# Kernel tuning notes

Hardware: AMD Instinct MI355X
Metric: run time of the kernel (lower is better)

The kernel has to match this reference:

```python
import jax, jax.numpy as jnp
import numpy as np

B, N, D, H, L = 2, 2048, 128, 8, 3
V = 32          # NUM_ATOM_TYPES (assumed)
DH = D // H
SCALE = 1.0 / (DH ** 0.5)
NEG = -1e9      # stands in for -inf in the additive attention mask
EPS = 1e-5


def _ln(x, g, b):
    m = x.mean(-1, keepdims=True)
    v = ((x - m) ** 2).mean(-1, keepdims=True)
    return (x - m) / jnp.sqrt(v + EPS) * g + b


def setup_inputs() -> dict:
    key = jax.random.key(0)
    ks = jax.random.split(key, 24)
    nrm = lambda k, shape, std=0.02: jax.random.normal(k, shape, jnp.float32) * std
    atom_embed = nrm(ks[0], (V, D)).at[0].set(0.0)  # padding_idx = 0
    cons_embed = nrm(ks[1], (1, 1, D))
    in_w = nrm(ks[2], (D, D)); in_b = jnp.zeros((D,), jnp.float32)
    qkv_w = nrm(ks[3], (L, 3 * D, D)); qkv_b = jnp.zeros((L, 3 * D), jnp.float32)
    out_w = nrm(ks[4], (L, D, D)); out_b = jnp.zeros((L, D), jnp.float32)
    ln1_g = jnp.ones((L, D), jnp.float32); ln1_b = jnp.zeros((L, D), jnp.float32)
    ln2_g = jnp.ones((L, D), jnp.float32); ln2_b = jnp.zeros((L, D), jnp.float32)
    ff1_w = nrm(ks[5], (L, 4 * D, D)); ff1_b = jnp.zeros((L, 4 * D), jnp.float32)
    ff2_w = nrm(ks[6], (L, D, 4 * D)); ff2_b = jnp.zeros((L, D), jnp.float32)
    struct_bias = nrm(ks[7], (L,), 0.5)  # scalar per layer (init 0 in torch; randomized to exercise the path)
    head_ln_g = jnp.ones((D,), jnp.float32); head_ln_b = jnp.zeros((D,), jnp.float32)
    head_w = nrm(ks[8], (1, D)); head_b = jnp.zeros((1,), jnp.float32)
    is_atom = jax.random.bernoulli(ks[9], 0.5, (B, N))
    atom_id = jax.random.randint(ks[10], (B, N), 0, V)
    mask = jax.random.bernoulli(ks[11], 0.9, (B, N))
    adjacency = (jax.random.uniform(ks[12], (B, N, N)) < 0.002).astype(jnp.float32)
    adjacency = jnp.maximum(adjacency, jnp.eye(N, dtype=jnp.float32)[None])  # self-loops
    root_idx = jax.random.randint(ks[13], (B,), 0, N)
    return dict(atom_embed=atom_embed, cons_embed=cons_embed, in_w=in_w, in_b=in_b,
                qkv_w=qkv_w, qkv_b=qkv_b, out_w=out_w, out_b=out_b,
                ln1_g=ln1_g, ln1_b=ln1_b, ln2_g=ln2_g, ln2_b=ln2_b,
                ff1_w=ff1_w, ff1_b=ff1_b, ff2_w=ff2_w, ff2_b=ff2_b,
                struct_bias=struct_bias, head_ln_g=head_ln_g, head_ln_b=head_ln_b,
                head_w=head_w, head_b=head_b, adjacency=adjacency,
                is_atom=is_atom, atom_id=atom_id, mask=mask, root_idx=root_idx)


def reference(atom_embed, cons_embed, in_w, in_b, qkv_w, qkv_b, out_w, out_b,
              ln1_g, ln1_b, ln2_g, ln2_b, ff1_w, ff1_b, ff2_w, ff2_b,
              struct_bias, head_ln_g, head_ln_b, head_w, head_b,
              adjacency, is_atom, atom_id, mask, root_idx):
    # node embeddings
    ae = atom_embed[jnp.clip(atom_id, 0, V - 1)]                     # [B,N,D]
    h = jnp.where(is_atom[..., None], ae, jnp.broadcast_to(cons_embed, (B, N, D)))
    h = h @ in_w.T + in_b
    # additive attention mask: valid pairs OK; invalid query rows attend only to self
    pair_ok = mask[:, :, None] & mask[:, None, :]
    eye = jnp.eye(N, dtype=bool)[None]
    ok = pair_ok | ((~mask)[:, :, None] & eye)
    am = jnp.where(ok, 0.0, NEG).astype(jnp.float32)                 # [B,N,N]
    for i in range(L):
        x = _ln(h, ln1_g[i], ln1_b[i])
        qkv = (x @ qkv_w[i].T + qkv_b[i]).reshape(B, N, 3, H, DH)
        q, k, v = (jnp.transpose(qkv[:, :, j], (0, 2, 1, 3)) for j in range(3))  # [B,H,N,DH]
        scores = jnp.einsum('bhqd,bhkd->bhqk', q, k) * SCALE \
                 + struct_bias[i] * adjacency[:, None] + am[:, None]
        attn = jax.nn.softmax(scores, axis=-1)
        o = jnp.einsum('bhqk,bhkd->bhqd', attn, v)
        o = jnp.transpose(o, (0, 2, 1, 3)).reshape(B, N, D)
        h = h + (o @ out_w[i].T + out_b[i])
        x2 = _ln(h, ln2_g[i], ln2_b[i])
        f = jax.nn.gelu(x2 @ ff1_w[i].T + ff1_b[i], approximate=False)
        h = h + (f @ ff2_w[i].T + ff2_b[i])
    pooled = h[jnp.arange(B), root_idx]                              # [B,D]
    p = _ln(pooled, head_ln_g, head_ln_b)
    return (p @ head_w.T + head_b)[:, 0]                             # [B]
```

## Files before the change

### kernel.cpp

```cpp
#include <hip/hip_runtime.h>
#include <cmath>

#define NB 2
#define NN 2048
#define ND 128
#define NH 8
#define NL 3
#define NV 32
#define NDH 16
#define LN_EPS 1e-5f
#define QSCALE 0.36067376022224085f

typedef __bf16 bf8_t __attribute__((ext_vector_type(8)));
typedef __bf16 bf4_t __attribute__((ext_vector_type(4)));
typedef float f4x __attribute__((ext_vector_type(4)));
typedef float f16x __attribute__((ext_vector_type(16)));

struct CastArgs {
  const float* s[5];
  __bf16* d[5];
  int startblk[5];
};
__global__ __launch_bounds__(256) void prep_kernel(
    CastArgs a, const float* __restrict__ adj, unsigned long long* __restrict__ abits,
    const int* __restrict__ mask, unsigned long long* __restrict__ mbits) {
  int blk = blockIdx.x;
  int lane = threadIdx.x & 63;
  if (blk < 592) {
    int seg = 0;
#pragma unroll
    for (int i = 1; i < 5; i++) seg += (blk >= a.startblk[i]) ? 1 : 0;
    int i4 = (blk - a.startblk[seg]) * 256 + threadIdx.x;
    float4 v = ((const float4*)a.s[seg])[i4];
    bf4_t p = {(__bf16)v.x, (__bf16)v.y, (__bf16)v.z, (__bf16)v.w};
    ((bf4_t*)a.d[seg])[i4] = p;
  } else if (blk < 592 + 8192) {
    int g = ((blk - 592) * 4 + (threadIdx.x >> 6)) * 4;
    const float* p = adj + (size_t)g * 64 + lane;
    unsigned long long w0 = __ballot(p[0] != 0.0f);
    unsigned long long w1 = __ballot(p[64] != 0.0f);
    unsigned long long w2 = __ballot(p[128] != 0.0f);
    unsigned long long w3 = __ballot(p[192] != 0.0f);
    if (lane == 0) {
      abits[g] = w0; abits[g + 1] = w1; abits[g + 2] = w2; abits[g + 3] = w3;
    }
  } else {
    int g = (blk - 8784) * 4 + (threadIdx.x >> 6);
    int v = mask[g * 64 + lane];
    unsigned long long bal = __ballot(v != 0);
    if (lane == 0) mbits[g] = bal;
  }
}

__global__ __launch_bounds__(512) void fused0_kernel(
    const float* __restrict__ atom_embed, const float* __restrict__ cons_embed,
    const int* __restrict__ is_atom, const int* __restrict__ atom_id,
    const __bf16* __restrict__ W1, const float* __restrict__ b1,
    float* __restrict__ Hout,
    const float* __restrict__ lng, const float* __restrict__ lnb,
    const __bf16* __restrict__ W2, const float* __restrict__ b2,
    __bf16* __restrict__ Qb, __bf16* __restrict__ Kb, __bf16* __restrict__ Vt) {
  __shared__ __bf16 Xs[16][136];
  __shared__ __bf16 Ws[128][136];
  __shared__ float Hs[16][132];
  __shared__ __bf16 X2[16][136];
  int m0 = blockIdx.x * 16;
  int g = blockIdx.y;
  int t = threadIdx.x;
  int lane = t & 63, w = t >> 6;
  int l15 = lane & 15, quad = lane >> 4;
  const int NC2 = (g == 0) ? 2 : 1;
  const int T = 1 + NC2;

  {
    int r = t >> 5, c = t & 31;
    int row = m0 + r;
    int id = atom_id[row];
    id = id < 0 ? 0 : (id > NV - 1 ? NV - 1 : id);
    const float* src = is_atom[row] ? (atom_embed + (size_t)id * ND) : cons_embed;
    float4 v = *(const float4*)&src[c * 4];
    bf4_t p = {(__bf16)v.x, (__bf16)v.y, (__bf16)v.z, (__bf16)v.w};
    *(bf4_t*)&Xs[r][c * 4] = p;
  }

  bf8_t wreg[4];
  auto issue = [&](int i) {
    const __bf16* base;
    int rowoff;
    if (i == 0) { base = W1; rowoff = 0; }
    else {
      int nc = (g == 0) ? (i - 1) : 2;
      base = W2; rowoff = nc * 128;
    }
#pragma unroll
    for (int jj = 0; jj < 4; jj++) {
      int c = t + jj * 512;
      wreg[jj] = *(const bf8_t*)&base[(size_t)(rowoff + (c >> 4)) * 128 + (c & 15) * 8];
    }
  };
  issue(0);

  for (int i = 0; i < T; i++) {
    if (i) __syncthreads();
#pragma unroll
    for (int jj = 0; jj < 4; jj++) {
      int c = t + jj * 512;
      *(bf8_t*)&Ws[c >> 4][(c & 15) * 8] = wreg[jj];
    }
    __syncthreads();
    if (i + 1 < T) issue(i + 1);
    if (i == 0) {
      f4x a1 = {0.f, 0.f, 0.f, 0.f};
#pragma unroll
      for (int kk = 0; kk < 4; kk++) {
        bf8_t a = *(const bf8_t*)&Xs[l15][kk * 32 + quad * 8];
        bf8_t b = *(const bf8_t*)&Ws[w * 16 + l15][kk * 32 + quad * 8];
        a1 = __builtin_amdgcn_mfma_f32_16x16x32_bf16(a, b, a1, 0, 0, 0);
      }
      int n = w * 16 + l15;
      float bv = b1[n];
#pragma unroll
      for (int r = 0; r < 4; r++) {
        int m = quad * 4 + r;
        float v = a1[r] + bv;
        if (g == 0) Hout[(size_t)(m0 + m) * ND + n] = v;
        Hs[m][n] = v;
      }
      __syncthreads();
      {
        int r = t >> 5, c = t & 31;
        float4 v = *(const float4*)&Hs[r][c * 4];
        float s1 = v.x + v.y + v.z + v.w;
        float s2 = v.x * v.x + v.y * v.y + v.z * v.z + v.w * v.w;
#pragma unroll
        for (int m = 16; m >= 1; m >>= 1) {
          s1 += __shfl_xor(s1, m, 64);
          s2 += __shfl_xor(s2, m, 64);
        }
        float mean = s1 * (1.0f / ND);
        float var = s2 * (1.0f / ND) - mean * mean;
        float rstd = rsqrtf(var + LN_EPS);
        float4 gg = *(const float4*)&lng[c * 4];
        float4 bb = *(const float4*)&lnb[c * 4];
        bf4_t p;
        p[0] = (__bf16)((v.x - mean) * rstd * gg.x + bb.x);
        p[1] = (__bf16)((v.y - mean) * rstd * gg.y + bb.y);
        p[2] = (__bf16)((v.z - mean) * rstd * gg.z + bb.z);
        p[3] = (__bf16)((v.w - mean) * rstd * gg.w + bb.w);
        *(bf4_t*)&X2[r][c * 4] = p;
      }
    } else {
      int nc = (g == 0) ? (i - 1) : 2;
      f4x a2 = {0.f, 0.f, 0.f, 0.f};
#pragma unroll
      for (int kk = 0; kk < 4; kk++) {
        bf8_t a = *(const bf8_t*)&X2[l15][kk * 32 + quad * 8];
        bf8_t b = *(const bf8_t*)&Ws[w * 16 + l15][kk * 32 + quad * 8];
        a2 = __builtin_amdgcn_mfma_f32_16x16x32_bf16(a, b, a2, 0, 0, 0);
      }
      int n = nc * 128 + w * 16 + l15;
      float bv = b2[n];
#pragma unroll
      for (int r = 0; r < 4; r++) {
        int m = m0 + quad * 4 + r;
        float v = a2[r] + bv;
        if (n < ND) Qb[(size_t)m * ND + n] = (__bf16)(v * QSCALE);
        else if (n < 2 * ND) Kb[(size_t)m * ND + n - ND] = (__bf16)v;
        else {
          int c2 = n - 2 * ND, hh = c2 >> 4, d0 = c2 & 15;
          int bb2 = m >> 11, nn = m & 2047;
          Vt[((size_t)((bb2 * NH + hh) * NDH + d0)) * NN + nn] = (__bf16)v;
        }
      }
    }
  }
}

template <int LAST>
__global__ __launch_bounds__(512) void layer_kernel(
    const __bf16* __restrict__ Ob,
    const __bf16* __restrict__ Wout, const float* __restrict__ bout,
    const float* __restrict__ Hin, float* __restrict__ Hout,
    const float* __restrict__ ln2g, const float* __restrict__ ln2b,
    const __bf16* __restrict__ Wff1, const float* __restrict__ bff1,
    const __bf16* __restrict__ Wff2, const float* __restrict__ bff2,
    const float* __restrict__ ln1g, const float* __restrict__ ln1b,
    const __bf16* __restrict__ Wqkv, const float* __restrict__ bqkv,
    __bf16* __restrict__ Qb, __bf16* __restrict__ Kb, __bf16* __restrict__ Vt,
    const int* __restrict__ root_idx, const float* __restrict__ hg,
    const float* __restrict__ hbt, const float* __restrict__ hwp,
    const float* __restrict__ hbp, float* __restrict__ outp) {
  __shared__ __bf16 Xs[16][136];
  __shared__ __bf16 Ws[128][136];
  __shared__ float Hs[16][132];
  __shared__ __bf16 X2[16][136];
  __shared__ __bf16 Fs[16][520];
  int m0 = blockIdx.x * 16;
  int g = blockIdx.y;
  int t = threadIdx.x;
  int lane = t & 63, w = t >> 6;
  int l15 = lane & 15, quad = lane >> 4;
  const int NQ = LAST ? 0 : (g == 0 ? 2 : 1);
  const int T = 9 + NQ;

  {
    int r = t >> 5, c = t & 31;
    *(bf4_t*)&Xs[r][c * 4] = *(const bf4_t*)&Ob[(size_t)(m0 + r) * ND + c * 4];
  }

  bf8_t wreg[4];
  auto issue = [&](int i) {
    const __bf16* base;
    int stride, rowoff, coloff;
    if (i == 0)     { base = Wout; stride = 128; rowoff = 0;             coloff = 0; }
    else if (i < 5) { base = Wff1; stride = 128; rowoff = (i - 1) * 128; coloff = 0; }
    else if (i < 9) { base = Wff2; stride = 512; rowoff = 0;             coloff = (i - 5) * 128; }
    else            { int nc = (g == 0) ? (i - 9) : 2;
                      base = Wqkv; stride = 128; rowoff = nc * 128;      coloff = 0; }
#pragma unroll
    for (int jj = 0; jj < 4; jj++) {
      int c = t + jj * 512;
      wreg[jj] = *(const bf8_t*)&base[(size_t)(rowoff + (c >> 4)) * stride + coloff + (c & 15) * 8];
    }
  };
  issue(0);

  auto do_ln = [&](const float* g_, const float* b_) {
    int r = t >> 5, c = t & 31;
    float4 v = *(const float4*)&Hs[r][c * 4];
    float s1 = v.x + v.y + v.z + v.w;
    float s2 = v.x * v.x + v.y * v.y + v.z * v.z + v.w * v.w;
#pragma unroll
    for (int m = 16; m >= 1; m >>= 1) {
      s1 += __shfl_xor(s1, m, 64);
      s2 += __shfl_xor(s2, m, 64);
    }
    float mean = s1 * (1.0f / ND);
    float var = s2 * (1.0f / ND) - mean * mean;
    float rstd = rsqrtf(var + LN_EPS);
    float4 gg = *(const float4*)&g_[c * 4];
    float4 bb = *(const float4*)&b_[c * 4];
    bf4_t p;
    p[0] = (__bf16)((v.x - mean) * rstd * gg.x + bb.x);
    p[1] = (__bf16)((v.y - mean) * rstd * gg.y + bb.y);
    p[2] = (__bf16)((v.z - mean) * rstd * gg.z + bb.z);
    p[3] = (__bf16)((v.w - mean) * rstd * gg.w + bb.w);
    *(bf4_t*)&X2[r][c * 4] = p;
  };

  f4x acc2 = {0.f, 0.f, 0.f, 0.f};
  for (int i = 0; i < T; i++) {
    if (i) __syncthreads();
#pragma unroll
    for (int jj = 0; jj < 4; jj++) {
      int c = t + jj * 512;
      *(bf8_t*)&Ws[c >> 4][(c & 15) * 8] = wreg[jj];
    }
    __syncthreads();
    if (i + 1 < T) issue(i + 1);
    if (i == 0) {
      f4x a1 = {0.f, 0.f, 0.f, 0.f};
#pragma unroll
      for (int kk = 0; kk < 4; kk++) {
        bf8_t a = *(const bf8_t*)&Xs[l15][kk * 32 + quad * 8];
        bf8_t b = *(const bf8_t*)&Ws[w * 16 + l15][kk * 32 + quad * 8];
        a1 = __builtin_amdgcn_mfma_f32_16x16x32_bf16(a, b, a1, 0, 0, 0);
      }
      int n = w * 16 + l15;
      float bv = bout[n];
#pragma unroll
      for (int r = 0; r < 4; r++) {
        int m = quad * 4 + r;
        Hs[m][n] = a1[r] + bv + Hin[(size_t)(m0 + m) * ND + n];
      }
      __syncthreads();
      do_ln(ln2g, ln2b);
    } else if (i < 5) {
      int c = i - 1;
      f4x a1 = {0.f, 0.f, 0.f, 0.f};
#pragma unroll
      for (int kk = 0; kk < 4; kk++) {
        bf8_t a = *(const bf8_t*)&X2[l15][kk * 32 + quad * 8];
        bf8_t b = *(const bf8_t*)&Ws[w * 16 + l15][kk * 32 + quad * 8];
        a1 = __builtin_amdgcn_mfma_f32_16x16x32_bf16(a, b, a1, 0, 0, 0);
      }
      int n = w * 16 + l15;
      float bv = bff1[c * 128 + n];
#pragma unroll
      for (int r = 0; r < 4; r++) {
        float v = a1[r] + bv;
        v = 0.5f * v * (1.0f + erff(v * 0.70710678118f));
        Fs[quad * 4 + r][c * 128 + n] = (__bf16)v;
      }
    } else if (i < 9) {
      int j = i - 5;
#pragma unroll
      for (int kk = 0; kk < 4; kk++) {
        bf8_t a = *(const bf8_t*)&Fs[l15][j * 128 + kk * 32 + quad * 8];
        bf8_t b = *(const bf8_t*)&Ws[w * 16 + l15][kk * 32 + quad * 8];
        acc2 = __builtin_amdgcn_mfma_f32_16x16x32_bf16(a, b, acc2, 0, 0, 0);
      }
      if (j == 3) {
        int n = w * 16 + l15;
        float bv = bff2[n];
#pragma unroll
        for (int r = 0; r < 4; r++) {
          int m = quad * 4 + r;
          float v = acc2[r] + bv + Hs[m][n];
          Hs[m][n] = v;
          if (g == 0) Hout[(size_t)(m0 + m) * ND + n] = v;
        }
        __syncthreads();
        if constexpr (!LAST) do_ln(ln1g, ln1b);
      }
    } else {
      int nc = (g == 0) ? (i - 9) : 2;
      f4x a2 = {0.f, 0.f, 0.f, 0.f};
#pragma unroll
      for (int kk = 0; kk < 4; kk++) {
        bf8_t a = *(const bf8_t*)&X2[l15][kk * 32 + quad * 8];
        bf8_t b = *(const bf8_t*)&Ws[w * 16 + l15][kk * 32 + quad * 8];
        a2 = __builtin_amdgcn_mfma_f32_16x16x32_bf16(a, b, a2, 0, 0, 0);
      }
      int n = nc * 128 + w * 16 + l15;
      float bv = bqkv[n];
#pragma unroll
      for (int r = 0; r < 4; r++) {
        int m = m0 + quad * 4 + r;
        float v = a2[r] + bv;
        if (n < ND) Qb[(size_t)m * ND + n] = (__bf16)(v * QSCALE);
        else if (n < 2 * ND) Kb[(size_t)m * ND + n - ND] = (__bf16)v;
        else {
          int c2 = n - 2 * ND, hh = c2 >> 4, d0 = c2 & 15;
          int bb2 = m >> 11, nn = m & 2047;
          Vt[((size_t)((bb2 * NH + hh) * NDH + d0)) * NN + nn] = (__bf16)v;
        }
      }
    }
  }

  if constexpr (LAST) {
    if (w < NB) {
      int rt = root_idx[w];
      int rglob = w * NN + rt;
      if (rglob >= m0 && rglob < m0 + 16) {
        int r = rglob - m0;
        float v0 = Hs[r][2 * lane], v1 = Hs[r][2 * lane + 1];
        float s1 = v0 + v1, s2 = v0 * v0 + v1 * v1;
#pragma unroll
        for (int m = 32; m >= 1; m >>= 1) {
          s1 += __shfl_xor(s1, m, 64);
          s2 += __shfl_xor(s2, m, 64);
        }
        float mean = s1 * (1.0f / ND);
        float var = s2 * (1.0f / ND) - mean * mean;
        float rstd = rsqrtf(var + LN_EPS);
        float p0 = (v0 - mean) * rstd * hg[2 * lane] + hbt[2 * lane];
        float p1 = (v1 - mean) * rstd * hg[2 * lane + 1] + hbt[2 * lane + 1];
        float part = p0 * hwp[2 * lane] + p1 * hwp[2 * lane + 1];
#pragma unroll
        for (int m = 32; m >= 1; m >>= 1) part += __shfl_xor(part, m, 64);
        if (lane == 0) outp[w] = part + hbp[0];
      }
    }
  }
}

__global__ __launch_bounds__(512) void attn_kernel(
    const __bf16* __restrict__ Qb, const __bf16* __restrict__ Kb,
    const __bf16* __restrict__ Vt, const unsigned int* __restrict__ adjbits,
    const unsigned int* __restrict__ maskbits, const int* __restrict__ mask,
    const float* __restrict__ sbias, int layer, __bf16* __restrict__ o) {
  int b = blockIdx.z, hh = blockIdx.y, q0 = blockIdx.x * 32;
  int wave = threadIdx.x >> 6;
  int lane = threadIdx.x & 63;
  int l31 = lane & 31, hi = lane >> 5;
  int l15 = lane & 15, quad = lane >> 4;
  float esb = __expf(sbias[layer]);
  const int bN = b * NN;
  const int kw0 = wave * 256;

  __shared__ __bf16 Pbuf[8][32][40];
  __shared__ float Ored[8][32][17];
  __shared__ float Lred[8][32];

  bf8_t Qf = *(const bf8_t*)(Qb + (size_t)(bN + q0 + l31) * ND + hh * NDH + hi * 8);

  int q = q0 + l31;
  int mq = mask[bN + q];
  const unsigned int* adjp = adjbits + (size_t)(bN + q) * (NN / 32) + (kw0 >> 5);
  const unsigned int* mbp = maskbits + (bN + kw0) / 32;
  const __bf16* kp = Kb + (size_t)(bN + kw0 + l31) * ND + hh * NDH + hi * 8;
  const __bf16* vp = Vt + (size_t)((b * NH + hh) * NDH + l15) * NN + kw0 + quad * 8;

  int dq = q - kw0;
  int tsel = dq >> 5;
  unsigned int selfw = 1u << (dq & 31);
  int sh4 = hi * 4;

  f4x Olo = {0.f, 0.f, 0.f, 0.f}, Ohi = {0.f, 0.f, 0.f, 0.f};
  float ls = 0.f;

  bf8_t Kf = *(const bf8_t*)kp;
  bf8_t Vf = *(const bf8_t*)vp;
  unsigned int aw = adjp[0];
  unsigned int mkw = mbp[0];

  for (int t = 0; t < 8; t++) {
    bf8_t Kn = Kf, Vn = Vf;
    unsigned int awn = aw, mkn = mkw;
    if (t < 7) {
      kp += 32 * ND;
      Kn = *(const bf8_t*)kp;
      Vn = *(const bf8_t*)(vp + (t + 1) * 32);
      awn = adjp[t + 1];
      mkn = mbp[t + 1];
    }
    f16x S = {0.f, 0.f, 0.f, 0.f, 0.f, 0.f, 0.f, 0.f,
              0.f, 0.f, 0.f, 0.f, 0.f, 0.f, 0.f, 0.f};
    S = __builtin_amdgcn_mfma_f32_32x32x16_bf16(Kf, Qf, S, 0, 0, 0);
    unsigned int okw = mq ? mkw : ((t == tsel) ? selfw : 0u);
    unsigned int wa = (aw & okw) >> sh4;
    unsigned int okh = okw >> sh4;
#pragma unroll
    for (int gg = 0; gg < 4; gg++) {
      bf4_t pk;
#pragma unroll
      for (int r = 0; r < 4; r++) {
        int c = gg * 8 + r;
        float e = __builtin_amdgcn_exp2f(S[gg * 4 + r]);
        float wgt = ((wa >> c) & 1) ? esb : (((okh >> c) & 1) ? 1.0f : 0.0f);
        float p = e * wgt;
        ls += p;
        pk[r] = (__bf16)p;
      }
      *(bf4_t*)&Pbuf[wave][l31][sh4 + gg * 8] = pk;
    }
    asm volatile("s_waitcnt lgkmcnt(0)" ::: "memory");
    bf8_t Plo = *(const bf8_t*)&Pbuf[wave][l15][quad * 8];
    bf8_t Phi = *(const bf8_t*)&Pbuf[wave][16 + l15][quad * 8];
    Olo = __builtin_amdgcn_mfma_f32_16x16x32_bf16(Plo, Vf, Olo, 0, 0, 0);
    Ohi = __builtin_amdgcn_mfma_f32_16x16x32_bf16(Phi, Vf, Ohi, 0, 0, 0);
    Kf = Kn; Vf = Vn; aw = awn; mkw = mkn;
  }

  ls += __shfl_xor(ls, 32, 64);
  if (hi == 0) Lred[wave][l31] = ls;
#pragma unroll
  for (int r = 0; r < 4; r++) {
    Ored[wave][quad * 4 + r][l15] = Olo[r];
    Ored[wave][16 + quad * 4 + r][l15] = Ohi[r];
  }
  __syncthreads();
  int row = threadIdx.x >> 4, col = threadIdx.x & 15;
  float s = 0.f, L = 0.f;
#pragma unroll
  for (int p = 0; p < 8; p++) {
    s += Ored[p][row][col];
    L += Lred[p][row];
  }
  o[(size_t)(bN + q0 + row) * ND + hh * NDH + col] = (__bf16)(s / L);
}

extern "C" void kernel_launch(void* const* d_in, const int* in_sizes, int n_in,
                              void* d_out, int out_size, void* d_ws, size_t ws_size,
                              hipStream_t stream) {
  const float* atom_embed = (const float*)d_in[0];
  const float* cons_embed = (const float*)d_in[1];
  const float* in_w  = (const float*)d_in[2];
  const float* in_b  = (const float*)d_in[3];
  const float* qkv_w = (const float*)d_in[4];
  const float* qkv_b = (const float*)d_in[5];
  const float* out_w = (const float*)d_in[6];
  const float* out_b = (const float*)d_in[7];
  const float* ln1_g = (const float*)d_in[8];
  const float* ln1_b = (const float*)d_in[9];
// ... 17 lines not shown

  const int MR = NB * NN;
  float* hA = (float*)d_ws;
  float* hB = hA + MR * ND;
  __bf16* Qb   = (__bf16*)(hB + MR * ND);
  __bf16* Kb   = Qb + MR * ND;
  __bf16* Vt   = Kb + MR * ND;
  __bf16* wbin = Vt + MR * ND;
  __bf16* wbqkv= wbin + ND * ND;
  __bf16* wbout= wbqkv + NL * 384 * ND;
  __bf16* wbff1= wbout + NL * ND * ND;
  __bf16* wbff2= wbff1 + NL * 512 * ND;
  unsigned int* adjb = (unsigned int*)(wbff2 + NL * ND * 512);
  unsigned int* mskb = adjb + NB * NN * NN / 32;
  __bf16* ob = (__bf16*)(mskb + 128);

  CastArgs ca;
  ca.s[0] = in_w;  ca.d[0] = wbin;  ca.startblk[0] = 0;
  ca.s[1] = qkv_w; ca.d[1] = wbqkv; ca.startblk[1] = 16;
  ca.s[2] = out_w; ca.d[2] = wbout; ca.startblk[2] = 160;
  ca.s[3] = ff1_w; ca.d[3] = wbff1; ca.startblk[3] = 208;
  ca.s[4] = ff2_w; ca.d[4] = wbff2; ca.startblk[4] = 400;
  prep_kernel<<<8800, 256, 0, stream>>>(ca, adj, (unsigned long long*)adjb,
                                        mask, (unsigned long long*)mskb);

  fused0_kernel<<<dim3(MR / 16, 2), 512, 0, stream>>>(
      atom_embed, cons_embed, is_atom, atom_id,
      wbin, in_b, hA, ln1_g, ln1_b, wbqkv, qkv_b, Qb, Kb, Vt);

  const float* hin[3]  = {hA, hB, hA};
  float* hout[3]       = {hB, hA, hB};
  for (int i = 0; i < NL; i++) {
    attn_kernel<<<dim3(NN / 32, NH, NB), 512, 0, stream>>>(
        Qb, Kb, Vt, adjb, mskb, mask, sbias, i, ob);
    if (i < NL - 1) {
      layer_kernel<0><<<dim3(MR / 16, 2), 512, 0, stream>>>(
          ob, wbout + (size_t)i * ND * ND, out_b + i * ND, hin[i], hout[i],
          ln2_g + i * ND, ln2_b + i * ND,
          wbff1 + (size_t)i * 512 * ND, ff1_b + i * 512,
          wbff2 + (size_t)i * ND * 512, ff2_b + i * ND,
          ln1_g + (i + 1) * ND, ln1_b + (i + 1) * ND,
          wbqkv + (size_t)(i + 1) * 384 * ND, qkv_b + (i + 1) * 384,
          Qb, Kb, Vt,
          nullptr, nullptr, nullptr, nullptr, nullptr, nullptr);
    } else {
      layer_kernel<1><<<dim3(MR / 16, 1), 512, 0, stream>>>(
          ob, wbout + (size_t)i * ND * ND, out_b + i * ND, hin[i], hout[i],
          ln2_g + i * ND, ln2_b + i * ND,
          wbff1 + (size_t)i * 512 * ND, ff1_b + i * 512,
          wbff2 + (size_t)i * ND * 512, ff2_b + i * ND,
          nullptr, nullptr, nullptr, nullptr,
          nullptr, nullptr, nullptr,
          root_idx, hg, hbt, hw, hb, out);
    }
  }
}
```

Before: 261.6 us.

## Fuse all layer kernels into one persistent megakernel with grid barriers

Replaces the separate fused0, attention and per-layer MLP kernel launches with a single persistent kernel of 512 blocks. The stages are separated by software grid barriers built on atomic counters, which prep_kernel zeroes. Each block handles two attention tiles and its share of the row-wise GEMM work per phase, reusing one dynamic shared memory buffer. The aim is to remove launch overhead and the gaps between kernels. The cost is barrier spin time, co-residency assumptions (512 blocks must all be resident), and possibly lower occupancy per phase.

Result: slower. 575.8 us (+120.1%).

```diff
diff --git a/kernel.cpp b/kernel.cpp
--- a/kernel.cpp
+++ b/kernel.cpp
@@ -10,6 +10,8 @@
 #define NDH 16
 #define LN_EPS 1e-5f
 #define QSCALE 0.36067376022224085f
+#define NBLK 512
+#define SMEM_BYTES 68608
 
 typedef __bf16 bf8_t __attribute__((ext_vector_type(8)));
 typedef __bf16 bf4_t __attribute__((ext_vector_type(4)));
@@ -23,9 +25,11 @@
 };
 __global__ __launch_bounds__(256) void prep_kernel(
     CastArgs a, const float* __restrict__ adj, unsigned long long* __restrict__ abits,
-    const int* __restrict__ mask, unsigned long long* __restrict__ mbits) {
+    const int* __restrict__ mask, unsigned long long* __restrict__ mbits,
+    unsigned* __restrict__ bars) {
   int blk = blockIdx.x;
   int lane = threadIdx.x & 63;
+  if (blk == 0 && threadIdx.x < 16) bars[threadIdx.x] = 0u;
   if (blk < 592) {
     int seg = 0;
 #pragma unroll
@@ -52,178 +56,56 @@
   }
 }
 
-__global__ __launch_bounds__(512) void fused0_kernel(
-    const float* __restrict__ atom_embed, const float* __restrict__ cons_embed,
-    const int* __restrict__ is_atom, const int* __restrict__ atom_id,
-    const __bf16* __restrict__ W1, const float* __restrict__ b1,
-    float* __restrict__ Hout,
-    const float* __restrict__ lng, const float* __restrict__ lnb,
-    const __bf16* __restrict__ W2, const float* __restrict__ b2,
-    __bf16* __restrict__ Qb, __bf16* __restrict__ Kb, __bf16* __restrict__ Vt) {
-  __shared__ __bf16 Xs[16][136];
-  __shared__ __bf16 Ws[128][136];
-  __shared__ float Hs[16][132];
-  __shared__ __bf16 X2[16][136];
-  int m0 = blockIdx.x * 16;
-  int g = blockIdx.y;
-  int t = threadIdx.x;
-  int lane = t & 63, w = t >> 6;
-  int l15 = lane & 15, quad = lane >> 4;
-  const int NC2 = (g == 0) ? 2 : 1;
-  const int T = 1 + NC2;
-
-  {
-    int r = t >> 5, c = t & 31;
-    int row = m0 + r;
-    int id = atom_id[row];
-    id = id < 0 ? 0 : (id > NV - 1 ? NV - 1 : id);
-    const float* src = is_atom[row] ? (atom_embed + (size_t)id * ND) : cons_embed;
-    float4 v = *(const float4*)&src[c * 4];
-    bf4_t p = {(__bf16)v.x, (__bf16)v.y, (__bf16)v.z, (__bf16)v.w};
-    *(bf4_t*)&Xs[r][c * 4] = p;
-  }
-
-  bf8_t wreg[4];
-  auto issue = [&](int i) {
-    const __bf16* base;
-    int rowoff;
-    if (i == 0) { base = W1; rowoff = 0; }
-    else {
-      int nc = (g == 0) ? (i - 1) : 2;
-      base = W2; rowoff = nc * 128;
-    }
-#pragma unroll
-    for (int jj = 0; jj < 4; jj++) {
-      int c = t + jj * 512;
-      wreg[jj] = *(const bf8_t*)&base[(size_t)(rowoff + (c >> 4)) * 128 + (c & 15) * 8];
-    }
+struct MegaArgs {
+  const float* atom_embed; const float* cons_embed;
+  const int* is_atom; const int* atom_id;
+  const __bf16* wbin; const float* in_b;
+  const __bf16* wbqkv; const float* qkv_b;
+  const __bf16* wbout; const float* out_b;
+  const __bf16* wbff1; const float* ff1_b;
+  const __bf16* wbff2; const float* ff2_b;
+  const float* ln1_g; const float* ln1_b;
+  const float* ln2_g; const float* ln2_b;
+  const float* sbias;
+  const float* hg; const float* hbt; const float* hw; const float* hb;
+  const int* root_idx; const int* mask;
+  const unsigned* adjb; const unsigned* mskb;
+  float* hA; float* hB;
+  __bf16* Qb; __bf16* Kb; __bf16* Vt; __bf16* ob;
+  unsigned* bars; float* out;
+};
+
+__global__ __launch_bounds__(512, 4) void mega_kernel(MegaArgs A) {
+  extern __shared__ char smem[];
+  const int blk = blockIdx.x;
+  const int t = threadIdx.x;
+  const int lane = t & 63, w = t >> 6;
+  const int l15 = lane & 15, quad = lane >> 4;
+
+  auto Xs = (__bf16(*)[136])(smem);
+  auto Ws = (__bf16(*)[136])(smem + 4352);
+  auto Hs = (float(*)[132])(smem + 39168);
+  auto X2 = (__bf16(*)[136])(smem + 47616);
+  auto Fs = (__bf16(*)[520])(smem + 51968);
+  auto Pbuf = (__bf16(*)[32][40])(smem);
+  auto Ored = (float(*)[32][17])(smem + 20480);
+  auto Lred = (float(*)[32])(smem + 37888);
+
+  auto gridbar = [&](int bi) {
+    __syncthreads();
+    if (t == 0) {
+      __threadfence();
+      unsigned old = atomicAdd(&A.bars[bi * 2], 1u);
+      if (old == NBLK - 1) {
+        atomicAdd(&A.bars[bi * 2 + 1], 1u);
+      } else {
+        while (atomicAdd(&A.bars[bi * 2 + 1], 0u) == 0u)
+          __builtin_amdgcn_s_sleep(2);
+      }
+      __threadfence();
+    }
+    __syncthreads();
   };
-  issue(0);
-
-  for (int i = 0; i < T; i++) {
-    if (i) __syncthreads();
-#pragma unroll
-    for (int jj = 0; jj < 4; jj++) {
-      int c = t + jj * 512;
-      *(bf8_t*)&Ws[c >> 4][(c & 15) * 8] = wreg[jj];
-    }
-    __syncthreads();
-    if (i + 1 < T) issue(i + 1);
-    if (i == 0) {
-      f4x a1 = {0.f, 0.f, 0.f, 0.f};
-#pragma unroll
-      for (int kk = 0; kk < 4; kk++) {
-        bf8_t a = *(const bf8_t*)&Xs[l15][kk * 32 + quad * 8];
-        bf8_t b = *(const bf8_t*)&Ws[w * 16 + l15][kk * 32 + quad * 8];
-        a1 = __builtin_amdgcn_mfma_f32_16x16x32_bf16(a, b, a1, 0, 0, 0);
-      }
-      int n = w * 16 + l15;
-      float bv = b1[n];
-#pragma unroll
-      for (int r = 0; r < 4; r++) {
-        int m = quad * 4 + r;
-        float v = a1[r] + bv;
-        if (g == 0) Hout[(size_t)(m0 + m) * ND + n] = v;
-        Hs[m][n] = v;
-      }
-      __syncthreads();
-      {
-        int r = t >> 5, c = t & 31;
-        float4 v = *(const float4*)&Hs[r][c * 4];
-        float s1 = v.x + v.y + v.z + v.w;
-        float s2 = v.x * v.x + v.y * v.y + v.z * v.z + v.w * v.w;
-#pragma unroll
-        for (int m = 16; m >= 1; m >>= 1) {
-          s1 += __shfl_xor(s1, m, 64);
-          s2 += __shfl_xor(s2, m, 64);
-        }
-        float mean = s1 * (1.0f / ND);
-        float var = s2 * (1.0f / ND) - mean * mean;
-        float rstd = rsqrtf(var + LN_EPS);
-        float4 gg = *(const float4*)&lng[c * 4];
-        float4 bb = *(const float4*)&lnb[c * 4];
-        bf4_t p;
-        p[0] = (__bf16)((v.x - mean) * rstd * gg.x + bb.x);
-        p[1] = (__bf16)((v.y - mean) * rstd * gg.y + bb.y);
-        p[2] = (__bf16)((v.z - mean) * rstd * gg.z + bb.z);
-        p[3] = (__bf16)((v.w - mean) * rstd * gg.w + bb.w);
-        *(bf4_t*)&X2[r][c * 4] = p;
-      }
-    } else {
-      int nc = (g == 0) ? (i - 1) : 2;
-      f4x a2 = {0.f, 0.f, 0.f, 0.f};
-#pragma unroll
-      for (int kk = 0; kk < 4; kk++) {
-        bf8_t a = *(const bf8_t*)&X2[l15][kk * 32 + quad * 8];
-        bf8_t b = *(const bf8_t*)&Ws[w * 16 + l15][kk * 32 + quad * 8];
-        a2 = __builtin_amdgcn_mfma_f32_16x16x32_bf16(a, b, a2, 0, 0, 0);
-      }
-      int n = nc * 128 + w * 16 + l15;
-      float bv = b2[n];
-#pragma unroll
-      for (int r = 0; r < 4; r++) {
-        int m = m0 + quad * 4 + r;
-        float v = a2[r] + bv;
-        if (n < ND) Qb[(size_t)m * ND + n] = (__bf16)(v * QSCALE);
-        else if (n < 2 * ND) Kb[(size_t)m * ND + n - ND] = (__bf16)v;
-        else {
-          int c2 = n - 2 * ND, hh = c2 >> 4, d0 = c2 & 15;
-          int bb2 = m >> 11, nn = m & 2047;
-          Vt[((size_t)((bb2 * NH + hh) * NDH + d0)) * NN + nn] = (__bf16)v;
-        }
-      }
-    }
-  }
-}
-
-template <int LAST>
-__global__ __launch_bounds__(512) void layer_kernel(
-    const __bf16* __restrict__ Ob,
-    const __bf16* __restrict__ Wout, const float* __restrict__ bout,
-    const float* __restrict__ Hin, float* __restrict__ Hout,
-    const float* __restrict__ ln2g, const float* __restrict__ ln2b,
-    const __bf16* __restrict__ Wff1, const float* __restrict__ bff1,
-    const __bf16* __restrict__ Wff2, const float* __restrict__ bff2,
-    const float* __restrict__ ln1g, const float* __restrict__ ln1b,
-    const __bf16* __restrict__ Wqkv, const float* __restrict__ bqkv,
-    __bf16* __restrict__ Qb, __bf16* __restrict__ Kb, __bf16* __restrict__ Vt,
-    const int* __restrict__ root_idx, const float* __restrict__ hg,
-    const float* __restrict__ hbt, const float* __restrict__ hwp,
-    const float* __restrict__ hbp, float* __restrict__ outp) {
-  __shared__ __bf16 Xs[16][136];
-  __shared__ __bf16 Ws[128][136];
-  __shared__ float Hs[16][132];
-  __shared__ __bf16 X2[16][136];
-  __shared__ __bf16 Fs[16][520];
-  int m0 = blockIdx.x * 16;
-  int g = blockIdx.y;
-  int t = threadIdx.x;
-  int lane = t & 63, w = t >> 6;
-  int l15 = lane & 15, quad = lane >> 4;
-  const int NQ = LAST ? 0 : (g == 0 ? 2 : 1);
-  const int T = 9 + NQ;
-
-  {
-    int r = t >> 5, c = t & 31;
-    *(bf4_t*)&Xs[r][c * 4] = *(const bf4_t*)&Ob[(size_t)(m0 + r) * ND + c * 4];
-  }
-
-  bf8_t wreg[4];
-  auto issue = [&](int i) {
-    const __bf16* base;
-    int stride, rowoff, coloff;
-    if (i == 0)     { base = Wout; stride = 128; rowoff = 0;             coloff = 0; }
-    else if (i < 5) { base = Wff1; stride = 128; rowoff = (i - 1) * 128; coloff = 0; }
-    else if (i < 9) { base = Wff2; stride = 512; rowoff = 0;             coloff = (i - 5) * 128; }
-    else            { int nc = (g == 0) ? (i - 9) : 2;
-                      base = Wqkv; stride = 128; rowoff = nc * 128;      coloff = 0; }
-#pragma unroll
-    for (int jj = 0; jj < 4; jj++) {
-      int c = t + jj * 512;
-      wreg[jj] = *(const bf8_t*)&base[(size_t)(rowoff + (c >> 4)) * stride + coloff + (c & 15) * 8];
-    }
-  };
-  issue(0);
 
   auto do_ln = [&](const float* g_, const float* b_) {
     int r = t >> 5, c = t & 31;
@@ -248,218 +130,335 @@
     *(bf4_t*)&X2[r][c * 4] = p;
   };
 
-  f4x acc2 = {0.f, 0.f, 0.f, 0.f};
-  for (int i = 0; i < T; i++) {
-    if (i) __syncthreads();
-#pragma unroll
-    for (int jj = 0; jj < 4; jj++) {
-      int c = t + jj * 512;
-      *(bf8_t*)&Ws[c >> 4][(c & 15) * 8] = wreg[jj];
-    }
-    __syncthreads();
-    if (i + 1 < T) issue(i + 1);
-    if (i == 0) {
-      f4x a1 = {0.f, 0.f, 0.f, 0.f};
-#pragma unroll
-      for (int kk = 0; kk < 4; kk++) {
-        bf8_t a = *(const bf8_t*)&Xs[l15][kk * 32 + quad * 8];
-        bf8_t b = *(const bf8_t*)&Ws[w * 16 + l15][kk * 32 + quad * 8];
-        a1 = __builtin_amdgcn_mfma_f32_16x16x32_bf16(a, b, a1, 0, 0, 0);
-      }
-      int n = w * 16 + l15;
-      float bv = bout[n];
-#pragma unroll
-      for (int r = 0; r < 4; r++) {
-        int m = quad * 4 + r;
-        Hs[m][n] = a1[r] + bv + Hin[(size_t)(m0 + m) * ND + n];
+  {
+    int m0 = (blk >> 1) * 16;
+    int g = blk & 1;
+    const int NC2 = (g == 0) ? 2 : 1;
+    const int T = 1 + NC2;
+    {
+      int r = t >> 5, c = t & 31;
+      int row = m0 + r;
+      int id = A.atom_id[row];
+      id = id < 0 ? 0 : (id > NV - 1 ? NV - 1 : id);
+      const float* src = A.is_atom[row] ? (A.atom_embed + (size_t)id * ND) : A.cons_embed;
+      float4 v = *(const float4*)&src[c * 4];
+      bf4_t p = {(__bf16)v.x, (__bf16)v.y, (__bf16)v.z, (__bf16)v.w};
+      *(bf4_t*)&Xs[r][c * 4] = p;
+    }
+    bf8_t wreg[4];
+    auto issue = [&](int i) {
+      const __bf16* base;
+      int rowoff;
+      if (i == 0) { base = A.wbin; rowoff = 0; }
+      else { int nc = (g == 0) ? (i - 1) : 2; base = A.wbqkv; rowoff = nc * 128; }
+#pragma unroll
+      for (int jj = 0; jj < 4; jj++) {
+        int c = t + jj * 512;
+        wreg[jj] = *(const bf8_t*)&base[(size_t)(rowoff + (c >> 4)) * 128 + (c & 15) * 8];
+      }
+    };
+    issue(0);
+    for (int i = 0; i < T; i++) {
+      if (i) __syncthreads();
+#pragma unroll
+      for (int jj = 0; jj < 4; jj++) {
+        int c = t + jj * 512;
+        *(bf8_t*)&Ws[c >> 4][(c & 15) * 8] = wreg[jj];
       }
       __syncthreads();
-      do_ln(ln2g, ln2b);
-    } else if (i < 5) {
-      int c = i - 1;
-      f4x a1 = {0.f, 0.f, 0.f, 0.f};
-#pragma unroll
-      for (int kk = 0; kk < 4; kk++) {
-        bf8_t a = *(const bf8_t*)&X2[l15][kk * 32 + quad * 8];
-        bf8_t b = *(const bf8_t*)&Ws[w * 16 + l15][kk * 32 + quad * 8];
-        a1 = __builtin_amdgcn_mfma_f32_16x16x32_bf16(a, b, a1, 0, 0, 0);
-      }
-      int n = w * 16 + l15;
-      float bv = bff1[c * 128 + n];
-#pragma unroll
-      for (int r = 0; r < 4; r++) {
-        float v = a1[r] + bv;
-        v = 0.5f * v * (1.0f + erff(v * 0.70710678118f));
-        Fs[quad * 4 + r][c * 128 + n] = (__bf16)v;
-      }
-    } else if (i < 9) {
-      int j = i - 5;
-#pragma unroll
-      for (int kk = 0; kk < 4; kk++) {
-        bf8_t a = *(const bf8_t*)&Fs[l15][j * 128 + kk * 32 + quad * 8];
-        bf8_t b = *(const bf8_t*)&Ws[w * 16 + l15][kk * 32 + quad * 8];
-        acc2 = __builtin_amdgcn_mfma_f32_16x16x32_bf16(a, b, acc2, 0, 0, 0);
-      }
-      if (j == 3) {
+      if (i + 1 < T) issue(i + 1);
+      if (i == 0) {
+        f4x a1 = {0.f, 0.f, 0.f, 0.f};
+#pragma unroll
+        for (int kk = 0; kk < 4; kk++) {
+          bf8_t a = *(const bf8_t*)&Xs[l15][kk * 32 + quad * 8];
+          bf8_t b = *(const bf8_t*)&Ws[w * 16 + l15][kk * 32 + quad * 8];
+          a1 = __builtin_amdgcn_mfma_f32_16x16x32_bf16(a, b, a1, 0, 0, 0);
+        }
         int n = w * 16 + l15;
-        float bv = bff2[n];
+        float bv = A.in_b[n];
 #pragma unroll
         for (int r = 0; r < 4; r++) {
           int m = quad * 4 + r;
-          float v = acc2[r] + bv + Hs[m][n];
+          float v = a1[r] + bv;
+          if (g == 0) A.hA[(size_t)(m0 + m) * ND + n] = v;
           Hs[m][n] = v;
-          if (g == 0) Hout[(size_t)(m0 + m) * ND + n] = v;
         }
         __syncthreads();
-        if constexpr (!LAST) do_ln(ln1g, ln1b);
-      }
-    } else {
-      int nc = (g == 0) ? (i - 9) : 2;
-      f4x a2 = {0.f, 0.f, 0.f, 0.f};
-#pragma unroll
-      for (int kk = 0; kk < 4; kk++) {
-        bf8_t a = *(const bf8_t*)&X2[l15][kk * 32 + quad * 8];
-        bf8_t b = *(const bf8_t*)&Ws[w * 16 + l15][kk * 32 + quad * 8];
-        a2 = __builtin_amdgcn_mfma_f32_16x16x32_bf16(a, b, a2, 0, 0, 0);
-      }
-      int n = nc * 128 + w * 16 + l15;
-      float bv = bqkv[n];
+        do_ln(A.ln1_g, A.ln1_b);
+      } else {
+        int nc = (g == 0) ? (i - 1) : 2;
+        f4x a2 = {0.f, 0.f, 0.f, 0.f};
+#pragma unroll
+        for (int kk = 0; kk < 4; kk++) {
+          bf8_t a = *(const bf8_t*)&X2[l15][kk * 32 + quad * 8];
+          bf8_t b = *(const bf8_t*)&Ws[w * 16 + l15][kk * 32 + quad * 8];
+          a2 = __builtin_amdgcn_mfma_f32_16x16x32_bf16(a, b, a2, 0, 0, 0);
+        }
+        int n = nc * 128 + w * 16 + l15;
+        float bv = A.qkv_b[n];
+#pragma unroll
+        for (int r = 0; r < 4; r++) {
+          int m = m0 + quad * 4 + r;
+          float v = a2[r] + bv;
+          if (n < ND) A.Qb[(size_t)m * ND + n] = (__bf16)(v * QSCALE);
+          else if (n < 2 * ND) A.Kb[(size_t)m * ND + n - ND] = (__bf16)v;
+          else {
+            int c2 = n - 2 * ND, hh = c2 >> 4, d0 = c2 & 15;
+            int bb2 = m >> 11, nn = m & 2047;
+            A.Vt[((size_t)((bb2 * NH + hh) * NDH + d0)) * NN + nn] = (__bf16)v;
+          }
+        }
+      }
+    }
+  }
+  gridbar(0);
+
+  for (int layer = 0; layer < NL; layer++) {
+    float esb = __expf(A.sbias[layer]);
+    for (int u2 = 0; u2 < 2; u2++) {
+      int u = blk + u2 * NBLK;
+      int b = u >> 9, hh = (u >> 6) & 7, q0 = (u & 63) * 32;
+      int l31 = lane & 31, hi = lane >> 5;
+      const int bN = b * NN;
+      const int kw0 = w * 256;
+
+      bf8_t Qf = *(const bf8_t*)(A.Qb + (size_t)(bN + q0 + l31) * ND + hh * NDH + hi * 8);
+      int q = q0 + l31;
+      int mq = A.mask[bN + q];
+      const unsigned* adjp = A.adjb + (size_t)(bN + q) * (NN / 32) + (kw0 >> 5);
+      const unsigned* mbp = A.mskb + (bN + kw0) / 32;
+      const __bf16* kp = A.Kb + (size_t)(bN + kw0 + l31) * ND + hh * NDH + hi * 8;
+      const __bf16* vp = A.Vt + (size_t)((b * NH + hh) * NDH + l15) * NN + kw0 + quad * 8;
+
+      int dq = q - kw0;
+      int tsel = dq >> 5;
+      unsigned selfw = 1u << (dq & 31);
+      int sh4 = hi * 4;
+
+      f4x Olo = {0.f, 0.f, 0.f, 0.f}, Ohi = {0.f, 0.f, 0.f, 0.f};
+      float ls = 0.f;
+
+      bf8_t Kf = *(const bf8_t*)kp;
+      bf8_t Vf = *(const bf8_t*)vp;
+      unsigned aw = adjp[0];
+      unsigned mkw = mbp[0];
+
+      for (int tt = 0; tt < 8; tt++) {
+        bf8_t Kn = Kf, Vn = Vf;
+        unsigned awn = aw, mkn = mkw;
+        if (tt < 7) {
+          kp += 32 * ND;
+          Kn = *(const bf8_t*)kp;
+          Vn = *(const bf8_t*)(vp + (tt + 1) * 32);
+          awn = adjp[tt + 1];
+          mkn = mbp[tt + 1];
+        }
+        f16x S = {0.f, 0.f, 0.f, 0.f, 0.f, 0.f, 0.f, 0.f,
+                  0.f, 0.f, 0.f, 0.f, 0.f, 0.f, 0.f, 0.f};
+        S = __builtin_amdgcn_mfma_f32_32x32x16_bf16(Kf, Qf, S, 0, 0, 0);
+        unsigned okw = mq ? mkw : ((tt == tsel) ? selfw : 0u);
+        unsigned wa = (aw & okw) >> sh4;
+        unsigned okh = okw >> sh4;
+#pragma unroll
+        for (int gg = 0; gg < 4; gg++) {
+          bf4_t pk;
+#pragma unroll
+          for (int r = 0; r < 4; r++) {
+            int c = gg * 8 + r;
+            float e = __builtin_amdgcn_exp2f(S[gg * 4 + r]);
+            float wgt = ((wa >> c) & 1) ? esb : (((okh >> c) & 1) ? 1.0f : 0.0f);
+            float p = e * wgt;
+            ls += p;
+            pk[r] = (__bf16)p;
+          }
+          *(bf4_t*)&Pbuf[w][l31][sh4 + gg * 8] = pk;
+        }
+        asm volatile("s_waitcnt lgkmcnt(0)" ::: "memory");
+        bf8_t Plo = *(const bf8_t*)&Pbuf[w][l15][quad * 8];
+        bf8_t Phi = *(const bf8_t*)&Pbuf[w][16 + l15][quad * 8];
+        Olo = __builtin_amdgcn_mfma_f32_16x16x32_bf16(Plo, Vf, Olo, 0, 0, 0);
+        Ohi = __builtin_amdgcn_mfma_f32_16x16x32_bf16(Phi, Vf, Ohi, 0, 0, 0);
+        Kf = Kn; Vf = Vn; aw = awn; mkw = mkn;
+      }
+
+      ls += __shfl_xor(ls, 32, 64);
+      if (hi == 0) Lred[w][l31] = ls;
 #pragma unroll
       for (int r = 0; r < 4; r++) {
-        int m = m0 + quad * 4 + r;
-        float v = a2[r] + bv;
-        if (n < ND) Qb[(size_t)m * ND + n] = (__bf16)(v * QSCALE);
-        else if (n < 2 * ND) Kb[(size_t)m * ND + n - ND] = (__bf16)v;
-        else {
-          int c2 = n - 2 * ND, hh = c2 >> 4, d0 = c2 & 15;
-          int bb2 = m >> 11, nn = m & 2047;
-          Vt[((size_t)((bb2 * NH + hh) * NDH + d0)) * NN + nn] = (__bf16)v;
-        }
-      }
-    }
+        Ored[w][quad * 4 + r][l15] = Olo[r];
+        Ored[w][16 + quad * 4 + r][l15] = Ohi[r];
+      }
+      __syncthreads();
+      int row = t >> 4, col = t & 15;
+      float s = 0.f, L = 0.f;
+#pragma unroll
+      for (int p = 0; p < 8; p++) {
+        s += Ored[p][row][col];
+        L += Lred[p][row];
+      }
+      A.ob[(size_t)(bN + q0 + row) * ND + hh * NDH + col] = (__bf16)(s / L);
+      __syncthreads();
+    }
+    gridbar(1 + 2 * layer);
+
+    {
+      int m0 = (blk >> 1) * 16;
+      int g = blk & 1;
+      const int last = (layer == NL - 1);
+      const float* Hin = (layer & 1) ? A.hB : A.hA;
+      float* Hout = (layer & 1) ? A.hA : A.hB;
+      const __bf16* Wout = A.wbout + (size_t)layer * ND * ND;
+      const float* bout = A.out_b + layer * ND;
+      const __bf16* Wff1 = A.wbff1 + (size_t)layer * 512 * ND;
+      const float* bff1 = A.ff1_b + layer * 512;
+      const __bf16* Wff2 = A.wbff2 + (size_t)layer * ND * 512;
+      const float* bff2 = A.ff2_b + layer * ND;
+      const __bf16* Wqkv = A.wbqkv + (size_t)(layer + 1) * 384 * ND;
+      const float* bqkv = A.qkv_b + (layer + 1) * 384;
+      const float* ln1g = A.ln1_g + (layer + 1) * ND;
+      const float* ln1b = A.ln1_b + (layer + 1) * ND;
+      const int NQ = last ? 0 : (g == 0 ? 2 : 1);
+      const int T = 9 + NQ;
+
+      {
+        int r = t >> 5, c = t & 31;
+        *(bf4_t*)&Xs[r][c * 4] = *(const bf4_t*)&A.ob[(size_t)(m0 + r) * ND + c * 4];
+      }
+      bf8_t wreg[4];
+      auto issue = [&](int i) {
+        const __bf16* base;
+        int stride, rowoff, coloff;
+        if (i == 0)     { base = Wout; stride = 128; rowoff = 0;             coloff = 0; }
+        else if (i < 5) { base = Wff1; stride = 128; rowoff = (i - 1) * 128; coloff = 0; }
+        else if (i < 9) { base = Wff2; stride = 512; rowoff = 0;             coloff = (i - 5) * 128; }
+        else            { int nc = (g == 0) ? (i - 9) : 2;
+                          base = Wqkv; stride = 128; rowoff = nc * 128;      coloff = 0; }
+#pragma unroll
+        for (int jj = 0; jj < 4; jj++) {
+          int c = t + jj * 512;
+          wreg[jj] = *(const bf8_t*)&base[(size_t)(rowoff + (c >> 4)) * stride + coloff + (c & 15) * 8];
+        }
+      };
+      issue(0);
+
+      f4x acc2 = {0.f, 0.f, 0.f, 0.f};
+      for (int i = 0; i < T; i++) {
+        if (i) __syncthreads();
+#pragma unroll
+        for (int jj = 0; jj < 4; jj++) {
+          int c = t + jj * 512;
+          *(bf8_t*)&Ws[c >> 4][(c & 15) * 8] = wreg[jj];
+        }
+        __syncthreads();
+        if (i + 1 < T) issue(i + 1);
+        if (i == 0) {
+          f4x a1 = {0.f, 0.f, 0.f, 0.f};
+#pragma unroll
+          for (int kk = 0; kk < 4; kk++) {
+            bf8_t a = *(const bf8_t*)&Xs[l15][kk * 32 + quad * 8];
+            bf8_t b = *(const bf8_t*)&Ws[w * 16 + l15][kk * 32 + quad * 8];
+            a1 = __builtin_amdgcn_mfma_f32_16x16x32_bf16(a, b, a1, 0, 0, 0);
+          }
+          int n = w * 16 + l15;
+          float bv = bout[n];
+#pragma unroll
+          for (int r = 0; r < 4; r++) {
+            int m = quad * 4 + r;
+            Hs[m][n] = a1[r] + bv + Hin[(size_t)(m0 + m) * ND + n];
+          }
+          __syncthreads();
+          do_ln(A.ln2_g + layer * ND, A.ln2_b + layer * ND);
+        } else if (i < 5) {
+          int c = i - 1;
+          f4x a1 = {0.f, 0.f, 0.f, 0.f};
+#pragma unroll
+          for (int kk = 0; kk < 4; kk++) {
+            bf8_t a = *(const bf8_t*)&X2[l15][kk * 32 + quad * 8];
+            bf8_t b = *(const bf8_t*)&Ws[w * 16 + l15][kk * 32 + quad * 8];
+            a1 = __builtin_amdgcn_mfma_f32_16x16x32_bf16(a, b, a1, 0, 0, 0);
+          }
+          int n = w * 16 + l15;
+          float bv = bff1[c * 128 + n];
+#pragma unroll
+          for (int r = 0; r < 4; r++) {
+            float v = a1[r] + bv;
+            v = 0.5f * v * (1.0f + erff(v * 0.70710678118f));
+            Fs[quad * 4 + r][c * 128 + n] = (__bf16)v;
+          }
+        } else if (i < 9) {
+          int j = i - 5;
+#pragma unroll
+          for (int kk = 0; kk < 4; kk++) {
+            bf8_t a = *(const bf8_t*)&Fs[l15][j * 128 + kk * 32 + quad * 8];
+            bf8_t b = *(const bf8_t*)&Ws[w * 16 + l15][kk * 32 + quad * 8];
+            acc2 = __builtin_amdgcn_mfma_f32_16x16x32_bf16(a, b, acc2, 0, 0, 0);
+          }
+          if (j == 3) {
+            int n = w * 16 + l15;
+            float bv = bff2[n];
+#pragma unroll
+            for (int r = 0; r < 4; r++) {
+              int m = quad * 4 + r;
+              float v = acc2[r] + bv + Hs[m][n];
+              Hs[m][n] = v;
+              if (g == 0) Hout[(size_t)(m0 + m) * ND + n] = v;
+            }
+            __syncthreads();
+            if (!last) do_ln(ln1g, ln1b);
+          }
+        } else {
+          int nc = (g == 0) ? (i - 9) : 2;
+          f4x a2 = {0.f, 0.f, 0.f, 0.f};
+#pragma unroll
+          for (int kk = 0; kk < 4; kk++) {
+            bf8_t a = *(const bf8_t*)&X2[l15][kk * 32 + quad * 8];
+            bf8_t b = *(const bf8_t*)&Ws[w * 16 + l15][kk * 32 + quad * 8];
+            a2 = __builtin_amdgcn_mfma_f32_16x16x32_bf16(a, b, a2, 0, 0, 0);
+          }
+          int n = nc * 128 + w * 16 + l15;
+          float bv = bqkv[n];
+#pragma unroll
+          for (int r = 0; r < 4; r++) {
+            int m = m0 + quad * 4 + r;
+            float v = a2[r] + bv;
+            if (n < ND) A.Qb[(size_t)m * ND + n] = (__bf16)(v * QSCALE);
+            else if (n < 2 * ND) A.Kb[(size_t)m * ND + n - ND] = (__bf16)v;
+            else {
+              int c2 = n - 2 * ND, hh = c2 >> 4, d0 = c2 & 15;
+              int bb2 = m >> 11, nn = m & 2047;
+              A.Vt[((size_t)((bb2 * NH + hh) * NDH + d0)) * NN + nn] = (__bf16)v;
+            }
+          }
+        }
+      }
+
+      if (last && g == 0 && w < NB) {
+        int rt = A.root_idx[w];
+        int rglob = w * NN + rt;
+        if (rglob >= m0 && rglob < m0 + 16) {
+          int r = rglob - m0;
+          float v0 = Hs[r][2 * lane], v1 = Hs[r][2 * lane + 1];
+          float s1 = v0 + v1, s2 = v0 * v0 + v1 * v1;
+#pragma unroll
+          for (int m = 32; m >= 1; m >>= 1) {
+            s1 += __shfl_xor(s1, m, 64);
+            s2 += __shfl_xor(s2, m, 64);
+          }
+          float mean = s1 * (1.0f / ND);
+          float var = s2 * (1.0f / ND) - mean * mean;
+          float rstd = rsqrtf(var + LN_EPS);
+          float p0 = (v0 - mean) * rstd * A.hg[2 * lane] + A.hbt[2 * lane];
+          float p1 = (v1 - mean) * rstd * A.hg[2 * lane + 1] + A.hbt[2 * lane + 1];
+          float part = p0 * A.hw[2 * lane] + p1 * A.hw[2 * lane + 1];
+#pragma unroll
+          for (int m = 32; m >= 1; m >>= 1) part += __shfl_xor(part, m, 64);
+          if (lane == 0) A.out[w] = part + A.hb[0];
+        }
+      }
+    }
+    if (layer < NL - 1) gridbar(2 + 2 * layer);
   }
-
-  if constexpr (LAST) {
-    if (w < NB) {
-      int rt = root_idx[w];
-      int rglob = w * NN + rt;
-      if (rglob >= m0 && rglob < m0 + 16) {
-        int r = rglob - m0;
-        float v0 = Hs[r][2 * lane], v1 = Hs[r][2 * lane + 1];
-        float s1 = v0 + v1, s2 = v0 * v0 + v1 * v1;
-#pragma unroll
-        for (int m = 32; m >= 1; m >>= 1) {
-          s1 += __shfl_xor(s1, m, 64);
-          s2 += __shfl_xor(s2, m, 64);
-        }
-        float mean = s1 * (1.0f / ND);
-        float var = s2 * (1.0f / ND) - mean * mean;
-        float rstd = rsqrtf(var + LN_EPS);
-        float p0 = (v0 - mean) * rstd * hg[2 * lane] + hbt[2 * lane];
-        float p1 = (v1 - mean) * rstd * hg[2 * lane + 1] + hbt[2 * lane + 1];
-        float part = p0 * hwp[2 * lane] + p1 * hwp[2 * lane + 1];
-#pragma unroll
-        for (int m = 32; m >= 1; m >>= 1) part += __shfl_xor(part, m, 64);
-        if (lane == 0) outp[w] = part + hbp[0];
-      }
-    }
-  }
-}
-
-__global__ __launch_bounds__(512) void attn_kernel(
-    const __bf16* __restrict__ Qb, const __bf16* __restrict__ Kb,
-    const __bf16* __restrict__ Vt, const unsigned int* __restrict__ adjbits,
-    const unsigned int* __restrict__ maskbits, const int* __restrict__ mask,
-    const float* __restrict__ sbias, int layer, __bf16* __restrict__ o) {
-  int b = blockIdx.z, hh = blockIdx.y, q0 = blockIdx.x * 32;
-  int wave = threadIdx.x >> 6;
-  int lane = threadIdx.x & 63;
-  int l31 = lane & 31, hi = lane >> 5;
-  int l15 = lane & 15, quad = lane >> 4;
-  float esb = __expf(sbias[layer]);
-  const int bN = b * NN;
-  const int kw0 = wave * 256;
-
-  __shared__ __bf16 Pbuf[8][32][40];
-  __shared__ float Ored[8][32][17];
-  __shared__ float Lred[8][32];
-
-  bf8_t Qf = *(const bf8_t*)(Qb + (size_t)(bN + q0 + l31) * ND + hh * NDH + hi * 8);
-
-  int q = q0 + l31;
-  int mq = mask[bN + q];
-  const unsigned int* adjp = adjbits + (size_t)(bN + q) * (NN / 32) + (kw0 >> 5);
-  const unsigned int* mbp = maskbits + (bN + kw0) / 32;
-  const __bf16* kp = Kb + (size_t)(bN + kw0 + l31) * ND + hh * NDH + hi * 8;
-  const __bf16* vp = Vt + (size_t)((b * NH + hh) * NDH + l15) * NN + kw0 + quad * 8;
-
-  int dq = q - kw0;
-  int tsel = dq >> 5;
-  unsigned int selfw = 1u << (dq & 31);
-  int sh4 = hi * 4;
-
-  f4x Olo = {0.f, 0.f, 0.f, 0.f}, Ohi = {0.f, 0.f, 0.f, 0.f};
-  float ls = 0.f;
-
-  bf8_t Kf = *(const bf8_t*)kp;
-  bf8_t Vf = *(const bf8_t*)vp;
-  unsigned int aw = adjp[0];
-  unsigned int mkw = mbp[0];
-
-  for (int t = 0; t < 8; t++) {
-    bf8_t Kn = Kf, Vn = Vf;
-    unsigned int awn = aw, mkn = mkw;
-    if (t < 7) {
-      kp += 32 * ND;
-      Kn = *(const bf8_t*)kp;
-      Vn = *(const bf8_t*)(vp + (t + 1) * 32);
-      awn = adjp[t + 1];
-      mkn = mbp[t + 1];
-    }
-    f16x S = {0.f, 0.f, 0.f, 0.f, 0.f, 0.f, 0.f, 0.f,
-              0.f, 0.f, 0.f, 0.f, 0.f, 0.f, 0.f, 0.f};
-    S = __builtin_amdgcn_mfma_f32_32x32x16_bf16(Kf, Qf, S, 0, 0, 0);
-    unsigned int okw = mq ? mkw : ((t == tsel) ? selfw : 0u);
-    unsigned int wa = (aw & okw) >> sh4;
-    unsigned int okh = okw >> sh4;
-#pragma unroll
-    for (int gg = 0; gg < 4; gg++) {
-      bf4_t pk;
-#pragma unroll
-      for (int r = 0; r < 4; r++) {
-        int c = gg * 8 + r;
-        float e = __builtin_amdgcn_exp2f(S[gg * 4 + r]);
-        float wgt = ((wa >> c) & 1) ? esb : (((okh >> c) & 1) ? 1.0f : 0.0f);
-        float p = e * wgt;
-        ls += p;
-        pk[r] = (__bf16)p;
-      }
-      *(bf4_t*)&Pbuf[wave][l31][sh4 + gg * 8] = pk;
-    }
-    asm volatile("s_waitcnt lgkmcnt(0)" ::: "memory");
-    bf8_t Plo = *(const bf8_t*)&Pbuf[wave][l15][quad * 8];
-    bf8_t Phi = *(const bf8_t*)&Pbuf[wave][16 + l15][quad * 8];
-    Olo = __builtin_amdgcn_mfma_f32_16x16x32_bf16(Plo, Vf, Olo, 0, 0, 0);
-    Ohi = __builtin_amdgcn_mfma_f32_16x16x32_bf16(Phi, Vf, Ohi, 0, 0, 0);
-    Kf = Kn; Vf = Vn; aw = awn; mkw = mkn;
-  }
-
-  ls += __shfl_xor(ls, 32, 64);
-  if (hi == 0) Lred[wave][l31] = ls;
-#pragma unroll
-  for (int r = 0; r < 4; r++) {
-    Ored[wave][quad * 4 + r][l15] = Olo[r];
-    Ored[wave][16 + quad * 4 + r][l15] = Ohi[r];
-  }
-  __syncthreads();
-  int row = threadIdx.x >> 4, col = threadIdx.x & 15;
-  float s = 0.f, L = 0.f;
-#pragma unroll
-  for (int p = 0; p < 8; p++) {
-    s += Ored[p][row][col];
-    L += Lred[p][row];
-  }
-  o[(size_t)(bN + q0 + row) * ND + hh * NDH + col] = (__bf16)(s / L);
 }
 
 extern "C" void kernel_launch(void* const* d_in, const int* in_sizes, int n_in,
@@ -507,6 +506,7 @@
   unsigned int* adjb = (unsigned int*)(wbff2 + NL * ND * 512);
   unsigned int* mskb = adjb + NB * NN * NN / 32;
   __bf16* ob = (__bf16*)(mskb + 128);
+  unsigned* bars = (unsigned*)(ob + MR * ND);
 
   CastArgs ca;
   ca.s[0] = in_w;  ca.d[0] = wbin;  ca.startblk[0] = 0;
@@ -515,36 +515,24 @@
   ca.s[3] = ff1_w; ca.d[3] = wbff1; ca.startblk[3] = 208;
   ca.s[4] = ff2_w; ca.d[4] = wbff2; ca.startblk[4] = 400;
   prep_kernel<<<8800, 256, 0, stream>>>(ca, adj, (unsigned long long*)adjb,
-                                        mask, (unsigned long long*)mskb);
-
-  fused0_kernel<<<dim3(MR / 16, 2), 512, 0, stream>>>(
-      atom_embed, cons_embed, is_atom, atom_id,
-      wbin, in_b, hA, ln1_g, ln1_b, wbqkv, qkv_b, Qb, Kb, Vt);
-
-  const float* hin[3]  = {hA, hB, hA};
-  float* hout[3]       = {hB, hA, hB};
-  for (int i = 0; i < NL; i++) {
-    attn_kernel<<<dim3(NN / 32, NH, NB), 512, 0, stream>>>(
-        Qb, Kb, Vt, adjb, mskb, mask, sbias, i, ob);
-    if (i < NL - 1) {
-      layer_kernel<0><<<dim3(MR / 16, 2), 512, 0, stream>>>(
-          ob, wbout + (size_t)i * ND * ND, out_b + i * ND, hin[i], hout[i],
-          ln2_g + i * ND, ln2_b + i * ND,
-          wbff1 + (size_t)i * 512 * ND, ff1_b + i * 512,
-          wbff2 + (size_t)i * ND * 512, ff2_b + i * ND,
-          ln1_g + (i + 1) * ND, ln1_b + (i + 1) * ND,
-          wbqkv + (size_t)(i + 1) * 384 * ND, qkv_b + (i + 1) * 384,
-          Qb, Kb, Vt,
-          nullptr, nullptr, nullptr, nullptr, nullptr, nullptr);
-    } else {
-      layer_kernel<1><<<dim3(MR / 16, 1), 512, 0, stream>>>(
-          ob, wbout + (size_t)i * ND * ND, out_b + i * ND, hin[i], hout[i],
-          ln2_g + i * ND, ln2_b + i * ND,
-          wbff1 + (size_t)i * 512 * ND, ff1_b + i * 512,
-          wbff2 + (size_t)i * ND * 512, ff2_b + i * ND,
-          nullptr, nullptr, nullptr, nullptr,
-          nullptr, nullptr, nullptr,
-          root_idx, hg, hbt, hw, hb, out);
-    }
-  }
+                                        mask, (unsigned long long*)mskb, bars);
+
+  MegaArgs A;
+  A.atom_embed = atom_embed; A.cons_embed = cons_embed;
+  A.is_atom = is_atom; A.atom_id = atom_id;
+  A.wbin = wbin; A.in_b = in_b;
+  A.wbqkv = wbqkv; A.qkv_b = qkv_b;
+  A.wbout = wbout; A.out_b = out_b;
+  A.wbff1 = wbff1; A.ff1_b = ff1_b;
+  A.wbff2 = wbff2; A.ff2_b = ff2_b;
+  A.ln1_g = ln1_g; A.ln1_b = ln1_b;
+  A.ln2_g = ln2_g; A.ln2_b = ln2_b;
+  A.sbias = sbias;
+  A.hg = hg; A.hbt = hbt; A.hw = hw; A.hb = hb;
+  A.root_idx = root_idx; A.mask = mask;
+  A.adjb = adjb; A.mskb = mskb;
+  A.hA = hA; A.hB = hB;
+  A.Qb = Qb; A.Kb = Kb; A.Vt = Vt; A.ob = ob;
+  A.bars = bars; A.out = out;
+  mega_kernel<<<NBLK, 512, SMEM_BYTES, stream>>>(A);
 }
```
